# Kernel tuning notes

Hardware: AMD Instinct MI355X
Metric: run time of the kernel (lower is better)

## Reference

```python
import jax, jax.numpy as jnp
import numpy as np

B, N, K = 4, 4096, 16
EPS = 1e-12


def setup_inputs() -> dict:
    key = jax.random.key(0)
    k1, k2, k3 = jax.random.split(key, 3)
    ori = jax.random.normal(k1, (B, N, 3), dtype=jnp.float32)
    # adversarial cloud = original + small perturbation (realistic attack setting)
    adv = ori + 0.05 * jax.random.normal(k2, (B, N, 3), dtype=jnp.float32)
    nrm = jax.random.normal(k3, (B, N, 3), dtype=jnp.float32)
    nrm = nrm / (jnp.linalg.norm(nrm, axis=-1, keepdims=True) + EPS)  # unit normals
    return {"ori_pcs": ori, "adv_pcs": adv, "ori_normals": nrm, "k": K}


def _sqdist(a, b):
    # a: [B,N,3], b: [B,M,3] -> [B,N,M] squared euclidean distances (GEMM form)
    return ((a * a).sum(-1)[:, :, None] + (b * b).sum(-1)[:, None, :]
            - 2.0 * jnp.einsum('bnd,bmd->bnm', a, b))


def _gather_rows(pts, idx):
    # pts: [B,M,3], idx: [B,...] int -> [B,...,3]
    return jax.vmap(lambda p, i: p[i])(pts, idx)


def _kappa(pc, normals, k):
    # curvature proxy: mean |<normalized offset to kNN, normal>| per point -> [B,N]
    d = _sqdist(pc, pc)                       # [B,N,N]
    _, idx = jax.lax.top_k(-d, k + 1)         # nearest k+1 (incl. self)
    idx = idx[..., 1:]                        # drop self -> [B,N,k]
    nn = _gather_rows(pc, idx)                # [B,N,k,3]
    vec = nn - pc[:, :, None, :]
    vec = vec / (jnp.linalg.norm(vec, axis=-1, keepdims=True) + EPS)
    return jnp.abs(jnp.einsum('bnkd,bnd->bnk', vec, normals)).mean(-1)


def reference(ori_pcs, adv_pcs, ori_normals, k):
    # curvature of the clean cloud
    kappa_ori = _kappa(ori_pcs, ori_normals, k)            # [B,N]
    # adv points borrow the normal of their nearest original point
    d = _sqdist(adv_pcs, ori_pcs)                          # [B,N,N]
    nn_idx = jnp.argmin(d, axis=-1)                        # [B,N]
    adv_normals = _gather_rows(ori_normals, nn_idx)        # [B,N,3]
    kappa_adv = _kappa(adv_pcs, adv_normals, k)            # [B,N]
    # std of curvature over points (torch.std -> unbiased, ddof=1)
    std_ori = jnp.std(kappa_ori, axis=1, ddof=1)           # [B]
    std_adv = jnp.std(kappa_adv, axis=1, ddof=1)           # [B]
    return jnp.mean(jnp.abs(std_adv - std_ori))
```

## Files before the change

### kernel.cpp

```cpp
#include <hip/hip_runtime.h>
#include <math.h>

#define B_ 4
#define N_ 4096
#define K_ 16
#define WAVES 8
#define QPW 2
#define QPB (WAVES*QPW)
#define BPB (N_/QPB)
#define INF __builtin_huge_valf()

__device__ __forceinline__ float dpp_shr1_f(float x) {
    return __int_as_float(__builtin_amdgcn_update_dpp(
        __float_as_int(x), __float_as_int(x), 0x111, 0xF, 0xF, false));
}
__device__ __forceinline__ int dpp_shr1_i(int x) {
    return __builtin_amdgcn_update_dpp(x, x, 0x111, 0xF, 0xF, false);
}
__device__ __forceinline__ float readlane_f(float x, int l) {
    return __int_as_float(__builtin_amdgcn_readlane(__float_as_int(x), l));
}

__global__ __launch_bounds__(512, 6) void curv_argmin_kernel(
    const float* __restrict__ ori, const float* __restrict__ adv,
    int* __restrict__ nnidx)
{
    __shared__ float2 sxy[N_];
    __shared__ float  sz[N_];
    const int tid  = threadIdx.x;
    const int lane = tid & 63;
    const int w    = tid >> 6;
    const int b    = blockIdx.x >> 8;
    const int qb   = (blockIdx.x & 255) * QPB;

    const float* ob = ori + (size_t)b * (N_*3);
    const float* ab = adv + (size_t)b * (N_*3);
    for (int k = 0; k < N_/512; ++k) {
        int j = k*512 + tid;
        sxy[j] = make_float2(ob[3*j+0], ob[3*j+1]);
        sz[j]  = ob[3*j+2];
    }
    __syncthreads();

    for (int qi = 0; qi < QPW; ++qi) {
        const int n  = qb + w*QPW + qi;
        const float qx = ab[3*n+0], qy = ab[3*n+1], qz = ab[3*n+2];
        float dm = INF; int jm = 0;
        for (int t = 0; t < N_/64; ++t) {
            int j = t*64 + lane;
            float2 p = sxy[j]; float pz = sz[j];
            float dx = qx - p.x, dy = qy - p.y, dz = qz - pz;
            float d  = dx*dx + dy*dy + dz*dz;
            bool better = d < dm;
            dm = better ? d : dm;
            jm = better ? j : jm;
        }
        for (int s = 1; s < 64; s <<= 1) {
            float od = __shfl_xor(dm, s);
            int   oj = __shfl_xor(jm, s);
            if (od < dm || (od == dm && oj < jm)) { dm = od; jm = oj; }
        }
        if (lane == 0) nnidx[b*N_ + n] = jm;
    }
}

__global__ __launch_bounds__(512, 6) void curv_kappa_kernel(
    const float* __restrict__ ori, const float* __restrict__ adv,
    const float* __restrict__ nrm, const int* __restrict__ nnidx,
    double* __restrict__ acc)
{
    __shared__ float2 sxy[N_];
    __shared__ float  sz[N_];
    __shared__ double rs[WAVES], rss[WAVES];
    const int tid  = threadIdx.x;
    const int lane = tid & 63;
    const int w    = tid >> 6;
    const int blk  = blockIdx.x;
    const int job  = blk >> 10;
    const int b    = (blk >> 8) & 3;
    const int qb   = (blk & 255) * QPB;

    const float* pb = (job ? adv : ori) + (size_t)b * (N_*3);
    const float* nb = nrm + (size_t)b * (N_*3);
    for (int k = 0; k < N_/512; ++k) {
        int j = k*512 + tid;
        sxy[j] = make_float2(pb[3*j+0], pb[3*j+1]);
        sz[j]  = pb[3*j+2];
    }
    __syncthreads();

    double ws_s = 0.0, ws_ss = 0.0;
    for (int qi = 0; qi < QPW; ++qi) {
        const int n = qb + w*QPW + qi;
        const float2 qxy = sxy[n];
        const float  qz  = sz[n];
        int nn = n;
        if (job) nn = nnidx[b*N_ + n];
        const float nrx = nb[3*nn+0], nry = nb[3*nn+1], nrz = nb[3*nn+2];

        float d; int idx = lane;
        {
            float2 p = sxy[lane]; float pz = sz[lane];
            float dx = qxy.x - p.x, dy = qxy.y - p.y, dz = qz - pz;
            d = dx*dx + dy*dy + dz*dz;
            if (lane == n) d = INF;
        }
        #pragma unroll
        for (int k = 2; k <= 64; k <<= 1) {
            #pragma unroll
            for (int j = k >> 1; j > 0; j >>= 1) {
                float od = __shfl_xor(d, j);
                int   oi = __shfl_xor(idx, j);
                bool dirUp = ((lane & k) == 0);
                bool lower = ((lane & j) == 0);
                bool oless = (od < d);
                bool take  = (dirUp == lower) ? oless : !oless;
                if (take) { d = od; idx = oi; }
            }
        }
        float sd = d; int si = idx;
        float tau = readlane_f(sd, 15);
        const int selfT = n >> 6, selfL = n & 63;

        for (int t = 1; t < N_/64; ++t) {
            int j = t*64 + lane;
            float2 p = sxy[j]; float pz = sz[j];
            float dx = qxy.x - p.x, dy = qxy.y - p.y, dz = qz - pz;
            float dd = dx*dx + dy*dy + dz*dz;
            if (t == selfT && lane == selfL) dd = INF;
            unsigned long long mask = __ballot(dd < tau);
            if (mask) {
                do {
                    int src = __builtin_ctzll(mask);
                    mask &= mask - 1;
                    float v = readlane_f(dd, src);
                    int  vi = t*64 + src;
                    bool gt = (sd > v);
                    unsigned long long mg = __ballot(gt);
                    float usd = dpp_shr1_f(sd);
                    int   usi = dpp_shr1_i(si);
                    bool  pg  = ((mg << 1) >> lane) & 1ull;
                    sd = gt ? (pg ? usd : v ) : sd;
                    si = gt ? (pg ? usi : vi) : si;
                } while (mask);
                tau = readlane_f(sd, 15);
            }
        }

        float tl = 0.0f;
        if (lane < K_) {
            float2 p = sxy[si]; float pz = sz[si];
            float vx = p.x - qxy.x, vy = p.y - qxy.y, vz = pz - qz;
            float L  = sqrtf(vx*vx + vy*vy + vz*vz) + 1e-12f;
            tl = fabsf(vx*nrx + vy*nry + vz*nrz) / L;
        }
        tl += __shfl_xor(tl, 1);
        tl += __shfl_xor(tl, 2);
        tl += __shfl_xor(tl, 4);
        tl += __shfl_xor(tl, 8);
        if (lane == 0) {
            double kap = (double)tl * (1.0/16.0);
            ws_s  += kap;
            ws_ss += kap * kap;
        }
    }

    if (lane == 0) { rs[w] = ws_s; rss[w] = ws_ss; }
    __syncthreads();
    if (tid == 0) {
        double s = 0.0, ss = 0.0;
        #pragma unroll
        for (int i = 0; i < WAVES; ++i) { s += rs[i]; ss += rss[i]; }
        int row = job*4 + b;
        atomicAdd(&acc[row*2+0], s);
        atomicAdd(&acc[row*2+1], ss);
    }
}

__global__ void curv_finalize_kernel(const double* __restrict__ acc,
                                     float* __restrict__ out)
{
    if (threadIdx.x == 0 && blockIdx.x == 0) {
        double st[8];
        #pragma unroll
        for (int r = 0; r < 8; ++r) {
            double s   = acc[2*r+0];
            double ss  = acc[2*r+1];
            double var = (ss - s*s / (double)N_) / (double)(N_ - 1);
            st[r] = var > 0.0 ? sqrt(var) : 0.0;
        }
        double o = 0.0;
        #pragma unroll
        for (int bb = 0; bb < 4; ++bb) o += fabs(st[4+bb] - st[bb]);
        out[0] = (float)(o * 0.25);
    }
}

extern "C" void kernel_launch(void* const* d_in, const int* in_sizes, int n_in,
                              void* d_out, int out_size, void* d_ws, size_t ws_size,
                              hipStream_t stream)
{
    const float* ori = (const float*)d_in[0];
    const float* adv = (const float*)d_in[1];
    const float* nrm = (const float*)d_in[2];
    double* acc   = (double*)d_ws;
    int*    nnidx = (int*)((char*)d_ws + 128);
    float*  out   = (float*)d_out;

    hipMemsetAsync(acc, 0, 16 * sizeof(double), stream);
    curv_argmin_kernel<<<dim3(B_ * BPB), 512, 0, stream>>>(ori, adv, nnidx);
    curv_kappa_kernel<<<dim3(2 * B_ * BPB), 512, 0, stream>>>(ori, adv, nrm, nnidx, acc);
    curv_finalize_kernel<<<1, 64, 0, stream>>>(acc, out);
}
```

Measured before the change: 146.4 us.

## Process two queries per wave jointly with GEMM-form distances

Both kernels now handle a wave's two queries in a single pass over the shared-memory points, so each point load serves two distance computations. Distances are computed as |p|^2 - 2 q·p with FMAs, dropping the constant |q|^2 term, which keeps the ranking but changes rounding behaviour. The lane-bit test uses inverse_ballot when the compiler provides it. The goal is fewer LDS reads and more independent work per iteration, at the cost of more registers and less exact distance values.

```diff
diff --git a/kernel.cpp b/kernel.cpp
--- a/kernel.cpp
+++ b/kernel.cpp
@@ -5,8 +5,7 @@
 #define N_ 4096
 #define K_ 16
 #define WAVES 8
-#define QPW 2
-#define QPB (WAVES*QPW)
+#define QPB (WAVES*2)
 #define BPB (N_/QPB)
 #define INF __builtin_huge_valf()
 
@@ -21,18 +20,21 @@
     return __int_as_float(__builtin_amdgcn_readlane(__float_as_int(x), l));
 }
 
+#if __has_builtin(__builtin_amdgcn_inverse_ballot_w64)
+#define LANEBIT(m, lane) __builtin_amdgcn_inverse_ballot_w64(m)
+#else
+#define LANEBIT(m, lane) ((((m) >> (lane)) & 1ull) != 0)
+#endif
+
 __global__ __launch_bounds__(512, 6) void curv_argmin_kernel(
     const float* __restrict__ ori, const float* __restrict__ adv,
     int* __restrict__ nnidx)
 {
     __shared__ float2 sxy[N_];
     __shared__ float  sz[N_];
-    const int tid  = threadIdx.x;
-    const int lane = tid & 63;
-    const int w    = tid >> 6;
-    const int b    = blockIdx.x >> 8;
-    const int qb   = (blockIdx.x & 255) * QPB;
-
+    const int tid = threadIdx.x, lane = tid & 63, w = tid >> 6;
+    const int b  = blockIdx.x >> 8;
+    const int qb = (blockIdx.x & 255) * QPB;
     const float* ob = ori + (size_t)b * (N_*3);
     const float* ab = adv + (size_t)b * (N_*3);
     for (int k = 0; k < N_/512; ++k) {
@@ -42,26 +44,27 @@
     }
     __syncthreads();
 
-    for (int qi = 0; qi < QPW; ++qi) {
-        const int n  = qb + w*QPW + qi;
-        const float qx = ab[3*n+0], qy = ab[3*n+1], qz = ab[3*n+2];
-        float dm = INF; int jm = 0;
-        for (int t = 0; t < N_/64; ++t) {
-            int j = t*64 + lane;
-            float2 p = sxy[j]; float pz = sz[j];
-            float dx = qx - p.x, dy = qy - p.y, dz = qz - pz;
-            float d  = dx*dx + dy*dy + dz*dz;
-            bool better = d < dm;
-            dm = better ? d : dm;
-            jm = better ? j : jm;
-        }
-        for (int s = 1; s < 64; s <<= 1) {
-            float od = __shfl_xor(dm, s);
-            int   oj = __shfl_xor(jm, s);
-            if (od < dm || (od == dm && oj < jm)) { dm = od; jm = oj; }
-        }
-        if (lane == 0) nnidx[b*N_ + n] = jm;
-    }
+    const int n0 = qb + w*2, n1 = n0 + 1;
+    const float m2x0 = -2.f*ab[3*n0+0], m2y0 = -2.f*ab[3*n0+1], m2z0 = -2.f*ab[3*n0+2];
+    const float m2x1 = -2.f*ab[3*n1+0], m2y1 = -2.f*ab[3*n1+1], m2z1 = -2.f*ab[3*n1+2];
+
+    float dm0 = INF, dm1 = INF; int jm0 = 0, jm1 = 0;
+    for (int t = 0; t < N_/64; ++t) {
+        int j = t*64 + lane;
+        float2 p = sxy[j]; float pz = sz[j];
+        float pp = fmaf(pz,pz, fmaf(p.y,p.y, p.x*p.x));
+        float r0 = fmaf(pz,m2z0, fmaf(p.y,m2y0, fmaf(p.x,m2x0, pp)));
+        float r1 = fmaf(pz,m2z1, fmaf(p.y,m2y1, fmaf(p.x,m2x1, pp)));
+        if (r0 < dm0) { dm0 = r0; jm0 = j; }
+        if (r1 < dm1) { dm1 = r1; jm1 = j; }
+    }
+    for (int s = 1; s < 64; s <<= 1) {
+        float o0 = __shfl_xor(dm0, s); int a0 = __shfl_xor(jm0, s);
+        float o1 = __shfl_xor(dm1, s); int a1 = __shfl_xor(jm1, s);
+        if (o0 < dm0 || (o0 == dm0 && a0 < jm0)) { dm0 = o0; jm0 = a0; }
+        if (o1 < dm1 || (o1 == dm1 && a1 < jm1)) { dm1 = o1; jm1 = a1; }
+    }
+    if (lane == 0) { nnidx[b*N_+n0] = jm0; nnidx[b*N_+n1] = jm1; }
 }
 
 __global__ __launch_bounds__(512, 6) void curv_kappa_kernel(
@@ -72,16 +75,14 @@
     __shared__ float2 sxy[N_];
     __shared__ float  sz[N_];
     __shared__ double rs[WAVES], rss[WAVES];
-    const int tid  = threadIdx.x;
-    const int lane = tid & 63;
-    const int w    = tid >> 6;
-    const int blk  = blockIdx.x;
-    const int job  = blk >> 10;
-    const int b    = (blk >> 8) & 3;
-    const int qb   = (blk & 255) * QPB;
-
-    const float* pb = (job ? adv : ori) + (size_t)b * (N_*3);
-    const float* nb = nrm + (size_t)b * (N_*3);
+    const int tid = threadIdx.x, lane = tid & 63, w = tid >> 6;
+    const int blk = blockIdx.x;
+    const int job = blk >> 10;
+    const int b   = (blk >> 8) & 3;
+    const int qb  = (blk & 255) * QPB;
+
+    const float* pb = (job ? adv : ori) + (size_t)b*(N_*3);
+    const float* nb = nrm + (size_t)b*(N_*3);
     for (int k = 0; k < N_/512; ++k) {
         int j = k*512 + tid;
         sxy[j] = make_float2(pb[3*j+0], pb[3*j+1]);
@@ -89,83 +90,113 @@
     }
     __syncthreads();
 
-    double ws_s = 0.0, ws_ss = 0.0;
-    for (int qi = 0; qi < QPW; ++qi) {
-        const int n = qb + w*QPW + qi;
-        const float2 qxy = sxy[n];
-        const float  qz  = sz[n];
-        int nn = n;
-        if (job) nn = nnidx[b*N_ + n];
-        const float nrx = nb[3*nn+0], nry = nb[3*nn+1], nrz = nb[3*nn+2];
-
-        float d; int idx = lane;
+    const int n0 = qb + w*2, n1 = n0 + 1;
+    const float2 q0 = sxy[n0]; const float q0z = sz[n0];
+    const float2 q1 = sxy[n1]; const float q1z = sz[n1];
+    const float m2x0 = -2.f*q0.x, m2y0 = -2.f*q0.y, m2z0 = -2.f*q0z;
+    const float m2x1 = -2.f*q1.x, m2y1 = -2.f*q1.y, m2z1 = -2.f*q1z;
+
+    int nn0 = n0, nn1 = n1;
+    if (job) { nn0 = nnidx[b*N_+n0]; nn1 = nnidx[b*N_+n1]; }
+    const float nx0 = nb[3*nn0+0], ny0 = nb[3*nn0+1], nz0 = nb[3*nn0+2];
+    const float nx1 = nb[3*nn1+0], ny1 = nb[3*nn1+1], nz1 = nb[3*nn1+2];
+
+    const int selfT = n0 >> 6;
+
+    float r0, r1; int i0 = lane, i1 = lane;
+    {
+        float2 p = sxy[lane]; float pz = sz[lane];
+        float pp = fmaf(pz,pz, fmaf(p.y,p.y, p.x*p.x));
+        r0 = fmaf(pz,m2z0, fmaf(p.y,m2y0, fmaf(p.x,m2x0, pp)));
+        r1 = fmaf(pz,m2z1, fmaf(p.y,m2y1, fmaf(p.x,m2x1, pp)));
+        if (selfT == 0) {
+            if (lane == n0) r0 = INF;
+            if (lane == n1) r1 = INF;
+        }
+    }
+    #pragma unroll
+    for (int k = 2; k <= 64; k <<= 1) {
+        #pragma unroll
+        for (int j = k >> 1; j > 0; j >>= 1) {
+            bool sel = ((lane & k) == 0) == ((lane & j) == 0);
+            float o0 = __shfl_xor(r0, j); int a0 = __shfl_xor(i0, j);
+            float o1 = __shfl_xor(r1, j); int a1 = __shfl_xor(i1, j);
+            if ((o0 < r0) == sel) { r0 = o0; i0 = a0; }
+            if ((o1 < r1) == sel) { r1 = o1; i1 = a1; }
+        }
+    }
+    float sd0 = r0, sd1 = r1; int si0 = i0, si1 = i1;
+    float tau0 = readlane_f(sd0, 15), tau1 = readlane_f(sd1, 15);
+    const int selfL0 = n0 & 63, selfL1 = n1 & 63;
+
+    for (int t = 1; t < N_/64; ++t) {
+        int j = t*64 + lane;
+        float2 p = sxy[j]; float pz = sz[j];
+        float pp = fmaf(pz,pz, fmaf(p.y,p.y, p.x*p.x));
+        float d0 = fmaf(pz,m2z0, fmaf(p.y,m2y0, fmaf(p.x,m2x0, pp)));
+        float d1 = fmaf(pz,m2z1, fmaf(p.y,m2y1, fmaf(p.x,m2x1, pp)));
+        if (t == selfT) {
+            if (lane == selfL0) d0 = INF;
+            if (lane == selfL1) d1 = INF;
+        }
+        unsigned long long m0 = __ballot(d0 < tau0);
+        if (m0) {
+            do {
+                int src = __builtin_ctzll(m0); m0 &= m0 - 1;
+                float v = readlane_f(d0, src);
+                int  vi = t*64 + src;
+                bool gt = (sd0 > v);
+                unsigned long long mg = __ballot(gt);
+                float usd = dpp_shr1_f(sd0); int usi = dpp_shr1_i(si0);
+                bool pg = LANEBIT(mg << 1, lane);
+                sd0 = gt ? (pg ? usd : v ) : sd0;
+                si0 = gt ? (pg ? usi : vi) : si0;
+            } while (m0);
+            tau0 = readlane_f(sd0, 15);
+        }
+        unsigned long long m1 = __ballot(d1 < tau1);
+        if (m1) {
+            do {
+                int src = __builtin_ctzll(m1); m1 &= m1 - 1;
+                float v = readlane_f(d1, src);
+                int  vi = t*64 + src;
+                bool gt = (sd1 > v);
+                unsigned long long mg = __ballot(gt);
+                float usd = dpp_shr1_f(sd1); int usi = dpp_shr1_i(si1);
+                bool pg = LANEBIT(mg << 1, lane);
+                sd1 = gt ? (pg ? usd : v ) : sd1;
+                si1 = gt ? (pg ? usi : vi) : si1;
+            } while (m1);
+            tau1 = readlane_f(sd1, 15);
+        }
+    }
+
+    float tl0 = 0.0f, tl1 = 0.0f;
+    if (lane < K_) {
         {
-            float2 p = sxy[lane]; float pz = sz[lane];
-            float dx = qxy.x - p.x, dy = qxy.y - p.y, dz = qz - pz;
-            d = dx*dx + dy*dy + dz*dz;
-            if (lane == n) d = INF;
-        }
-        #pragma unroll
-        for (int k = 2; k <= 64; k <<= 1) {
-            #pragma unroll
-            for (int j = k >> 1; j > 0; j >>= 1) {
-                float od = __shfl_xor(d, j);
-                int   oi = __shfl_xor(idx, j);
-                bool dirUp = ((lane & k) == 0);
-                bool lower = ((lane & j) == 0);
-                bool oless = (od < d);
-                bool take  = (dirUp == lower) ? oless : !oless;
-                if (take) { d = od; idx = oi; }
-            }
-        }
-        float sd = d; int si = idx;
-        float tau = readlane_f(sd, 15);
-        const int selfT = n >> 6, selfL = n & 63;
-
-        for (int t = 1; t < N_/64; ++t) {
-            int j = t*64 + lane;
-            float2 p = sxy[j]; float pz = sz[j];
-            float dx = qxy.x - p.x, dy = qxy.y - p.y, dz = qz - pz;
-            float dd = dx*dx + dy*dy + dz*dz;
-            if (t == selfT && lane == selfL) dd = INF;
-            unsigned long long mask = __ballot(dd < tau);
-            if (mask) {
-                do {
-                    int src = __builtin_ctzll(mask);
-                    mask &= mask - 1;
-                    float v = readlane_f(dd, src);
-                    int  vi = t*64 + src;
-                    bool gt = (sd > v);
-                    unsigned long long mg = __ballot(gt);
-                    float usd = dpp_shr1_f(sd);
-                    int   usi = dpp_shr1_i(si);
-                    bool  pg  = ((mg << 1) >> lane) & 1ull;
-                    sd = gt ? (pg ? usd : v ) : sd;
-                    si = gt ? (pg ? usi : vi) : si;
-                } while (mask);
-                tau = readlane_f(sd, 15);
-            }
-        }
-
-        float tl = 0.0f;
-        if (lane < K_) {
-            float2 p = sxy[si]; float pz = sz[si];
-            float vx = p.x - qxy.x, vy = p.y - qxy.y, vz = pz - qz;
+            float2 p = sxy[si0]; float pz = sz[si0];
+            float vx = p.x - q0.x, vy = p.y - q0.y, vz = pz - q0z;
             float L  = sqrtf(vx*vx + vy*vy + vz*vz) + 1e-12f;
-            tl = fabsf(vx*nrx + vy*nry + vz*nrz) / L;
-        }
-        tl += __shfl_xor(tl, 1);
-        tl += __shfl_xor(tl, 2);
-        tl += __shfl_xor(tl, 4);
-        tl += __shfl_xor(tl, 8);
-        if (lane == 0) {
-            double kap = (double)tl * (1.0/16.0);
-            ws_s  += kap;
-            ws_ss += kap * kap;
-        }
-    }
-
-    if (lane == 0) { rs[w] = ws_s; rss[w] = ws_ss; }
+            tl0 = fabsf(vx*nx0 + vy*ny0 + vz*nz0) / L;
+        }
+        {
+            float2 p = sxy[si1]; float pz = sz[si1];
+            float vx = p.x - q1.x, vy = p.y - q1.y, vz = pz - q1z;
+            float L  = sqrtf(vx*vx + vy*vy + vz*vz) + 1e-12f;
+            tl1 = fabsf(vx*nx1 + vy*ny1 + vz*nz1) / L;
+        }
+    }
+    tl0 += __shfl_xor(tl0, 1); tl0 += __shfl_xor(tl0, 2);
+    tl0 += __shfl_xor(tl0, 4); tl0 += __shfl_xor(tl0, 8);
+    tl1 += __shfl_xor(tl1, 1); tl1 += __shfl_xor(tl1, 2);
+    tl1 += __shfl_xor(tl1, 4); tl1 += __shfl_xor(tl1, 8);
+
+    if (lane == 0) {
+        double k0 = (double)tl0 * (1.0/16.0);
+        double k1 = (double)tl1 * (1.0/16.0);
+        rs[w]  = k0 + k1;
+        rss[w] = k0*k0 + k1*k1;
+    }
     __syncthreads();
     if (tid == 0) {
         double s = 0.0, ss = 0.0;
```

Measured after the change: 117.3 us. 1.25x faster.
